# Optimization experiments

Hardware: AMD Instinct MI355X
Metric: run time of the kernel (lower is better)

Reference implementation:

```python
import jax, jax.numpy as jnp
import numpy as np

T, G = 8, 128                      # time frames, spatial grid per axis
RMIN, RMAX = -1.5, 1.5             # same range for x, y, z
STEP = (RMAX - RMIN) / G           # voxel step per axis
# corner order: [C000, C100, C010, C110, C001, C101, C011, C111]
_OFFSETS = jnp.array([[0,0,0],[1,0,0],[0,1,0],[1,1,0],
                      [0,0,1],[1,0,1],[0,1,1],[1,1,1]], dtype=jnp.int32)

def _trilinear_coef(p):
    # p: [N,3] fractional position inside the cell, in [0,1)
    u, v, w = p[:, 0], p[:, 1], p[:, 2]
    return jnp.stack([(1-u)*(1-v)*(1-w), u*(1-v)*(1-w), (1-u)*v*(1-w), u*v*(1-w),
                      (1-u)*(1-v)*w,     u*(1-v)*w,     (1-u)*v*w,     u*v*w], axis=1)

def setup_inputs() -> dict:
    key = jax.random.key(0)
    k1, k2, k3, k4 = jax.random.split(key, 4)
    N = 1048576
    pos = jax.random.uniform(k1, (N, 3), jnp.float32, RMIN, RMAX)
    t = jax.random.randint(k2, (N,), 0, T, dtype=jnp.int32)
    sigma = jax.random.uniform(k3, (N,), jnp.float32)
    target_norm = jax.random.normal(k4, (N, 3), jnp.float32)
    lr = jnp.full((1,), 0.1, jnp.float32)
    voxel_array = jnp.full((T, G, G, G, 3), jnp.sqrt(1.0 / 3.0), jnp.float32)
    return {"t": t, "pos": pos, "lr": lr, "sigma": sigma,
            "target_norm": target_norm, "voxel_array": voxel_array}

def reference(t, pos, lr, sigma, target_norm, voxel_array):
    # shift into [0, range) coords (all axes share the same range/step)
    pos_s = pos - RMIN
    min_idx = jnp.floor(pos_s / STEP).astype(jnp.int32)          # [N,3], == // in source
    idx = jnp.clip(min_idx[:, None, :] + _OFFSETS[None], 0, G - 1)  # [N,8,3]
    frac = jnp.mod(pos_s, STEP) / STEP                           # [N,3]
    coef = _trilinear_coef(frac)                                 # [N,8]
    xi, yi, zi = idx[..., 0], idx[..., 1], idx[..., 2]
    ti = jnp.broadcast_to(t[:, None], xi.shape)                  # [N,8]
    vertex_values = voxel_array[ti, xi, yi, zi]                  # [N,8,3] gather
    value = jnp.sum(coef[:, :, None] * vertex_values, axis=1)    # [N,3]
    # update weights
    sigma_weight = (1.0 - jnp.exp(-sigma))[:, None]              # [N,1]
    update_lambda = jax.nn.sigmoid(lr * sigma_weight * coef)[..., None]  # [N,8,1]
    new_vertex_values = update_lambda * target_norm[:, None, :] + (1.0 - update_lambda) * vertex_values
    diff = new_vertex_values - vertex_values                     # [N,8,3]
    new_voxel = voxel_array.at[ti.reshape(-1), xi.reshape(-1),
                               yi.reshape(-1), zi.reshape(-1)].add(diff.reshape(-1, 3))
    return value, new_voxel
```

## Files before the change

### kernel.cpp

```cpp
#include <hip/hip_runtime.h>
#include <hip/hip_fp16.h>
#include <math.h>


#define GRES 128
#define NBINS (8 * 128 * 128)
#define CAP 16
#define OVF_MAX 16384
#define SCAN_BLOCKS 512
constexpr float RMIN_F = -1.5f;
constexpr float STEP_F = 3.0f / 128.0f;

typedef float f32x4a4 __attribute__((ext_vector_type(4), aligned(4)));
typedef float f32x2a4 __attribute__((ext_vector_type(2), aligned(4)));

__device__ __forceinline__ float fast_sigmoid(float x) {
    if (__builtin_expect(fabsf(x) < 0.5f, 1)) {
        return fmaf(x, fmaf(x * x, -(1.0f / 48.0f), 0.25f), 0.5f);
    }
    return 1.0f / (1.0f + __expf(-x));
}

__device__ __forceinline__ uint4 make_payload(
    int i, float px, float py, float pz, int mz,
    const float* __restrict__ target, float lrsw)
{
    float u = fmodf(px, STEP_F) / STEP_F;
    float v = fmodf(py, STEP_F) / STEP_F;
    float w = fmodf(pz, STEP_F) / STEP_F;
    unsigned qu = (unsigned)(u * 2047.0f + 0.5f);
    unsigned qv = (unsigned)(v * 2047.0f + 0.5f);
    unsigned qw = (unsigned)(w * 1023.0f + 0.5f);
    unsigned hx = (unsigned)__half_as_ushort(__float2half(target[3 * i + 0]));
    unsigned hy = (unsigned)__half_as_ushort(__float2half(target[3 * i + 1]));
    unsigned hz = (unsigned)__half_as_ushort(__float2half(target[3 * i + 2]));
    unsigned hl = (unsigned)__half_as_ushort(__float2half(lrsw));
    uint4 p;
    p.x = (qu << 21) | (qv << 10) | qw;
    p.y = ((unsigned)i << 7) | (unsigned)mz;
    p.z = hx | (hy << 16);
    p.w = hz | (hl << 16);
    return p;
}

__global__ __launch_bounds__(256) void place_kernel(
    const int*   __restrict__ t,     const float* __restrict__ pos,
    const float* __restrict__ lr_p,  const float* __restrict__ sigma,
    const float* __restrict__ target,
    unsigned* __restrict__ hist,     uint4* __restrict__ bins,
    unsigned* __restrict__ ovfcnt,   unsigned* __restrict__ ovf_key,
    uint4*    __restrict__ ovf_pay,  int N)
{
    int i = blockIdx.x * blockDim.x + threadIdx.x;
    if (i >= N) return;
    float px = pos[3 * i + 0] - RMIN_F;
    float py = pos[3 * i + 1] - RMIN_F;
    float pz = pos[3 * i + 2] - RMIN_F;
    int cx = min((int)floorf(px / STEP_F), GRES - 1);
    int cy = min((int)floorf(py / STEP_F), GRES - 1);
    int mz = min((int)floorf(pz / STEP_F), GRES - 1);
    float lrsw = lr_p[0] * (1.0f - __expf(-sigma[i]));
    uint4 p = make_payload(i, px, py, pz, mz, target, lrsw);
    unsigned key  = ((unsigned)t[i] << 14) | ((unsigned)cx << 7) | (unsigned)cy;
    unsigned rank = atomicAdd(&hist[key], 1u);
    if (rank < CAP) {
        bins[(size_t)key * CAP + rank] = p;
    } else {
        unsigned o = atomicAdd(ovfcnt, 1u);
        if (o < OVF_MAX) { ovf_key[o] = key; ovf_pay[o] = p; }
    }
}

__global__ __launch_bounds__(256) void key_hist_kernel(
    const int* __restrict__ t, const float* __restrict__ pos,
    unsigned* __restrict__ keys, unsigned* __restrict__ hist, int N)
{
    int i = blockIdx.x * blockDim.x + threadIdx.x;
    if (i >= N) return;
    float px = pos[3 * i + 0] - RMIN_F;
    float py = pos[3 * i + 1] - RMIN_F;
    int cx = min((int)floorf(px / STEP_F), GRES - 1);
    int cy = min((int)floorf(py / STEP_F), GRES - 1);
    unsigned key  = ((unsigned)t[i] << 14) | ((unsigned)cx << 7) | (unsigned)cy;
    unsigned rank = atomicAdd(&hist[key], 1u);
    keys[i] = (key << 15) | rank;
}

__global__ __launch_bounds__(256) void scanA_kernel(
    const unsigned* __restrict__ hist, unsigned* __restrict__ binstart,
    unsigned* __restrict__ partial)
{
    __shared__ unsigned sh[256];
    const int tid = threadIdx.x;
    const int gid = blockIdx.x * 256 + tid;
    unsigned x = hist[gid];
    sh[tid] = x;
    __syncthreads();
    for (int off = 1; off < 256; off <<= 1) {
        unsigned v = (tid >= off) ? sh[tid - off] : 0u;
        __syncthreads();
        sh[tid] += v;
        __syncthreads();
    }
    binstart[gid] = sh[tid] - x;
    if (tid == 255) partial[blockIdx.x] = sh[255];
}

__global__ __launch_bounds__(256) void scanC_kernel(
    unsigned* __restrict__ binstart, const unsigned* __restrict__ partial, int N)
{
    __shared__ unsigned s_w[4];
    unsigned loc = 0;
    for (int i = threadIdx.x; i < blockIdx.x; i += 256) loc += partial[i];
    #pragma unroll
    for (int off = 32; off > 0; off >>= 1) loc += __shfl_down(loc, off);
    if ((threadIdx.x & 63) == 0) s_w[threadIdx.x >> 6] = loc;
    __syncthreads();
    const unsigned off0 = s_w[0] + s_w[1] + s_w[2] + s_w[3];
    const int gid = blockIdx.x * 256 + threadIdx.x;
    binstart[gid] += off0;
    if (gid == 0) binstart[NBINS] = (unsigned)N;
}

__global__ __launch_bounds__(256) void scatter_kernel(
    const float* __restrict__ pos, const float* __restrict__ lr_p,
    const float* __restrict__ sigma, const float* __restrict__ target,
    const unsigned* __restrict__ keys, const unsigned* __restrict__ binstart,
    uint4* __restrict__ sorted, int N)
{
    int i = blockIdx.x * blockDim.x + threadIdx.x;
    if (i >= N) return;
    unsigned kr   = keys[i];
    unsigned key  = kr >> 15;
    unsigned rank = kr & 0x7fffu;
    unsigned slot = binstart[key] + rank;
    float px = pos[3 * i + 0] - RMIN_F;
    float py = pos[3 * i + 1] - RMIN_F;
    float pz = pos[3 * i + 2] - RMIN_F;
    int   mz = min((int)floorf(pz / STEP_F), GRES - 1);
    float lrsw = lr_p[0] * (1.0f - __expf(-sigma[i]));
    sorted[slot] = make_payload(i, px, py, pz, mz, target, lrsw);
}

__device__ __forceinline__ void process_event(
    const uint4 p, const int cx, const int cy,
    const int x0, const int y0, const int z0, const size_t tbase,
    const float* __restrict__ voxel_in,
    float* __restrict__ out_value, float* __restrict__ s_acc)
{
    const float u = (float)(p.x >> 21)           * (1.0f / 2047.0f);
    const float v = (float)((p.x >> 10) & 2047u) * (1.0f / 2047.0f);
    const float w = (float)(p.x & 1023u)         * (1.0f / 1023.0f);
    const int  mz  = (int)(p.y & 127u);
    const int  idx = (int)(p.y >> 7);
    const float tx = __half2float(__ushort_as_half((unsigned short)(p.z & 0xffffu)));
    const float ty = __half2float(__ushort_as_half((unsigned short)(p.z >> 16)));
    const float tz = __half2float(__ushort_as_half((unsigned short)(p.w & 0xffffu)));
    const float lrsw = __half2float(__ushort_as_half((unsigned short)(p.w >> 16)));

    const int xs1 = min(cx + 1, GRES - 1);
    const int ys1 = min(cy + 1, GRES - 1);
    const int zs1 = min(mz + 1, GRES - 1);
    const int zb  = min(mz, GRES - 2);
    const bool ztop = (mz == GRES - 1);
    const int szl = mz  - z0;
    const int szh = zs1 - z0;

    float lo[4][3], hi[4][3];
    #pragma unroll
    for (int q = 0; q < 4; ++q) {
        const int xi = (q & 1) ? xs1 : cx;
        const int yi = (q & 2) ? ys1 : cy;
        const float* vp = voxel_in + tbase + (((size_t)xi * GRES + yi) * GRES + zb) * 3;
        f32x4a4 f0 = *(const f32x4a4*)vp;
        f32x2a4 f1 = *(const f32x2a4*)(vp + 4);
        hi[q][0] = f0.w; hi[q][1] = f1.x; hi[q][2] = f1.y;
        lo[q][0] = ztop ? f0.w : f0.x;
        lo[q][1] = ztop ? f1.x : f0.y;
        lo[q][2] = ztop ? f1.y : f0.z;
    }

    float c[8];
    c[0] = (1.f - u) * (1.f - v) * (1.f - w);
    c[1] =        u  * (1.f - v) * (1.f - w);
    c[2] = (1.f - u) *        v  * (1.f - w);
    c[3] =        u  *        v  * (1.f - w);
    c[4] = (1.f - u) * (1.f - v) *        w;
    c[5] =        u  * (1.f - v) *        w;
    c[6] = (1.f - u) *        v  *        w;
    c[7] =        u  *        v  *        w;

    const bool owner = (cx >= x0) && (cy >= y0);

    float vx = 0.f, vy = 0.f, vz = 0.f;
    #pragma unroll
    for (int q = 0; q < 4; ++q) {
        if (owner) {
            vx += c[q] * lo[q][0] + c[q + 4] * hi[q][0];
            vy += c[q] * lo[q][1] + c[q + 4] * hi[q][1];
            vz += c[q] * lo[q][2] + c[q + 4] * hi[q][2];
        }
        const int xi = (q & 1) ? xs1 : cx;
        const int yi = (q & 2) ? ys1 : cy;
        const int sxi = xi - x0, syi = yi - y0;
        if (sxi >= 0 && sxi < 4 && syi >= 0 && syi < 4) {
            const int col = (sxi * 4 + syi) * 64;
            if (szl >= 0 && szl < 64) {
                const float laml = fast_sigmoid(lrsw * c[q]);
                const int sal = (col + szl) * 3;
                atomicAdd(&s_acc[sal + 0], laml * (tx - lo[q][0]));
                atomicAdd(&s_acc[sal + 1], laml * (ty - lo[q][1]));
                atomicAdd(&s_acc[sal + 2], laml * (tz - lo[q][2]));
            }
            if (szh >= 0 && szh < 64) {
                const float lamh = fast_sigmoid(lrsw * c[q + 4]);
                const int sah = (col + szh) * 3;
                atomicAdd(&s_acc[sah + 0], lamh * (tx - hi[q][0]));
                atomicAdd(&s_acc[sah + 1], lamh * (ty - hi[q][1]));
                atomicAdd(&s_acc[sah + 2], lamh * (tz - hi[q][2]));
            }
        }
    }
    if (owner) {
        out_value[3 * idx + 0] = vx;
        out_value[3 * idx + 1] = vy;
        out_value[3 * idx + 2] = vz;
    }
}

__global__ __launch_bounds__(256, 8) void brick_kernel(
    const unsigned* __restrict__ counts,
    const uint4*    __restrict__ sorted,
    const float*    __restrict__ voxel_in,
    float*          __restrict__ out_value,
    float*          __restrict__ out_voxel,
    int cap,
    const unsigned* __restrict__ ovf_key,
    const uint4*    __restrict__ ovf_pay,
    const unsigned* __restrict__ ovfcnt)
{
    __shared__ __align__(16) float s_acc[4 * 4 * 64 * 3];
    __shared__ unsigned s_start[25];
    __shared__ unsigned s_pref[26];
    __shared__ unsigned s_novf;

    const int t  = blockIdx.x & 7;
    const int s  = blockIdx.x >> 3;
    const int bx = s >> 6;
    const int by = (s >> 1) & 31;
    const int zh = s & 1;
    const int x0 = bx << 2, y0 = by << 2, z0 = zh << 6;
    const int zlo = z0 ? z0 - 1 : 0;
    const int zhi = z0 + 63;
    const int tid = threadIdx.x;
    const size_t tbase = (size_t)t * (GRES * GRES * GRES * 3);

    float4* s_acc4 = (float4*)s_acc;
    for (int q = tid; q < 768; q += 256) s_acc4[q] = make_float4(0.f, 0.f, 0.f, 0.f);

    if (tid < 64) {
        unsigned st = 0, cnt = 0;
        if (tid < 25) {
            int dxb = tid / 5 - 1, dyb = tid % 5 - 1;
            int cx = x0 + dxb, cy = y0 + dyb;
            if (cx >= 0 && cx < GRES && cy >= 0 && cy < GRES) {
                unsigned key = ((unsigned)t << 14) | ((unsigned)cx << 7) | (unsigned)cy;
                if (cap > 0) {
                    st  = key * (unsigned)cap;
                    cnt = min(counts[key], (unsigned)cap);
                } else {
                    st  = counts[key];
                    cnt = counts[key + 1] - st;
                }
            }
            s_start[tid] = st;
        }
        unsigned x = cnt;
        #pragma unroll
        for (int off = 1; off < 32; off <<= 1) {
            unsigned y = __shfl_up(x, off);
            if (tid >= off) x += y;
        }
        if (tid < 25) s_pref[tid + 1] = x;
        if (tid == 0) s_pref[0] = 0;
    }
    if (tid == 64) s_novf = (cap > 0) ? *ovfcnt : 0u;
    __syncthreads();
    const int P = (int)s_pref[25];

    for (int j = tid; j < P; j += 256) {
        int b = 0;
        #pragma unroll
        for (int sh = 16; sh > 0; sh >>= 1) {
            int nb = b + sh;
            if (nb <= 24 && s_pref[nb] <= (unsigned)j) b = nb;
        }
        const int cx = x0 + b / 5 - 1, cy = y0 + b % 5 - 1;
        const unsigned g = s_start[b] + ((unsigned)j - s_pref[b]);
        const uint4 p = sorted[g];
        const int mz = (int)(p.y & 127u);
        if (mz < zlo || mz > zhi) continue;
        process_event(p, cx, cy, x0, y0, z0, tbase, voxel_in, out_value, s_acc);
    }

    if (cap > 0) {
        const unsigned novf = min(s_novf, (unsigned)OVF_MAX);
        for (unsigned o = tid; o < novf; o += 256) {
            const unsigned key = ovf_key[o];
            if ((int)(key >> 14) != t) continue;
            const int ocx = (int)((key >> 7) & 127u), ocy = (int)(key & 127u);
            const int dxb = ocx - x0, dyb = ocy - y0;
            if (dxb < -1 || dxb > 3 || dyb < -1 || dyb > 3) continue;
            const uint4 p = ovf_pay[o];
            const int mz = (int)(p.y & 127u);
            if (mz < zlo || mz > zhi) continue;
            process_event(p, ocx, ocy, x0, y0, z0, tbase, voxel_in, out_value, s_acc);
        }
    }
    __syncthreads();

    for (int q = tid; q < 768; q += 256) {
        int col = q / 48, r = q - col * 48;
        int ox = col >> 2, oy = col & 3;
        const size_t coff = tbase + (size_t)(x0 + ox) * 49152
                                  + (size_t)(y0 + oy) * 384 + (size_t)z0 * 3;
        float4 a = *((const float4*)(voxel_in + coff) + r);
        float4 d = s_acc4[q];
        *((float4*)(out_voxel + coff) + r) =
            make_float4(a.x + d.x, a.y + d.y, a.z + d.z, a.w + d.w);
    }
}

extern "C" void kernel_launch(void* const* d_in, const int* in_sizes, int n_in,
                              void* d_out, int out_size, void* d_ws, size_t ws_size,
                              hipStream_t stream) {
    const int*   t      = (const int*)  d_in[0];
    const float* pos    = (const float*)d_in[1];
    const float* lr     = (const float*)d_in[2];
    const float* sigma  = (const float*)d_in[3];
    const float* target = (const float*)d_in[4];
    const float* voxel  = (const float*)d_in[5];

    const int N = in_sizes[0];

    float* out_value = (float*)d_out;
    float* out_voxel = out_value + (size_t)3 * N;

    const int block = 256;
    const int grid  = (N + block - 1) / block;

    const size_t need = (size_t)NBINS * CAP * 16 + (size_t)NBINS * 4 + 64
                      + (size_t)OVF_MAX * 4 + (size_t)OVF_MAX * 16;

    if (ws_size >= need) {
        uint4*    bins    = (uint4*)d_ws;
        unsigned* hist    = (unsigned*)(bins + (size_t)NBINS * CAP);
        unsigned* ovfcnt  = hist + NBINS;
        unsigned* ovf_key = ovfcnt + 16;
        uint4*    ovf_pay = (uint4*)(ovf_key + OVF_MAX);

        hipMemsetAsync(hist, 0, NBINS * sizeof(unsigned) + 64, stream);
        place_kernel<<<grid, block, 0, stream>>>(t, pos, lr, sigma, target,
                                                 hist, bins, ovfcnt, ovf_key,
                                                 ovf_pay, N);
        brick_kernel<<<16384, 256, 0, stream>>>(hist, bins, voxel,
                                                out_value, out_voxel,
                                                CAP, ovf_key, ovf_pay, ovfcnt);
    } else {
        uint4*    sorted   = (uint4*)d_ws;
        unsigned* keys     = (unsigned*)(sorted + (size_t)N);
        unsigned* hist     = keys + N;
        unsigned* binstart = hist + NBINS;
        unsigned* partial  = binstart + (NBINS + 1);

        hipMemsetAsync(hist, 0, NBINS * sizeof(unsigned), stream);
        key_hist_kernel<<<grid, block, 0, stream>>>(t, pos, keys, hist, N);
        scanA_kernel<<<SCAN_BLOCKS, 256, 0, stream>>>(hist, binstart, partial);
        scanC_kernel<<<SCAN_BLOCKS, 256, 0, stream>>>(binstart, partial, N);
        scatter_kernel<<<grid, block, 0, stream>>>(pos, lr, sigma, target, keys,
                                                   binstart, sorted, N);
        brick_kernel<<<16384, 256, 0, stream>>>(binstart, sorted, voxel,
                                                out_value, out_voxel,
                                                0, nullptr, nullptr, nullptr);
    }
}
```

Measured before the change: 510.1 us.

## Bin by z-half with 4-byte slot payloads and reload inputs in brick kernel

Bins are split by z-half, so each brick reads only its own events, and events at the z boundary (mz==63) are placed in both halves. Instead of a 16-byte packed payload, each bin entry is now a 4-byte index+mz word. The brick kernel re-reads pos, target and sigma per event, which removes the quantisation and half-precision packing. The multi-kernel sort fallback and the workspace size check are removed, and nontemporal loads and stores are added. This trades smaller bin traffic and exact inputs for random gathers of input arrays in the brick kernel, and it now assumes the workspace is large enough.

After: 546.3 us. +7.1%, slower.

```diff
diff --git a/kernel.cpp b/kernel.cpp
--- a/kernel.cpp
+++ b/kernel.cpp
@@ -4,10 +4,9 @@
 
 
 #define GRES 128
-#define NBINS (8 * 128 * 128)
-#define CAP 16
-#define OVF_MAX 16384
-#define SCAN_BLOCKS 512
+#define NBINS2 (1 << 18)
+#define CAP 12
+#define OVF_MAX 8192
 constexpr float RMIN_F = -1.5f;
 constexpr float STEP_F = 3.0f / 128.0f;
 
@@ -21,35 +20,11 @@
     return 1.0f / (1.0f + __expf(-x));
 }
 
-__device__ __forceinline__ uint4 make_payload(
-    int i, float px, float py, float pz, int mz,
-    const float* __restrict__ target, float lrsw)
-{
-    float u = fmodf(px, STEP_F) / STEP_F;
-    float v = fmodf(py, STEP_F) / STEP_F;
-    float w = fmodf(pz, STEP_F) / STEP_F;
-    unsigned qu = (unsigned)(u * 2047.0f + 0.5f);
-    unsigned qv = (unsigned)(v * 2047.0f + 0.5f);
-    unsigned qw = (unsigned)(w * 1023.0f + 0.5f);
-    unsigned hx = (unsigned)__half_as_ushort(__float2half(target[3 * i + 0]));
-    unsigned hy = (unsigned)__half_as_ushort(__float2half(target[3 * i + 1]));
-    unsigned hz = (unsigned)__half_as_ushort(__float2half(target[3 * i + 2]));
-    unsigned hl = (unsigned)__half_as_ushort(__float2half(lrsw));
-    uint4 p;
-    p.x = (qu << 21) | (qv << 10) | qw;
-    p.y = ((unsigned)i << 7) | (unsigned)mz;
-    p.z = hx | (hy << 16);
-    p.w = hz | (hl << 16);
-    return p;
-}
-
 __global__ __launch_bounds__(256) void place_kernel(
-    const int*   __restrict__ t,     const float* __restrict__ pos,
-    const float* __restrict__ lr_p,  const float* __restrict__ sigma,
-    const float* __restrict__ target,
-    unsigned* __restrict__ hist,     uint4* __restrict__ bins,
-    unsigned* __restrict__ ovfcnt,   unsigned* __restrict__ ovf_key,
-    uint4*    __restrict__ ovf_pay,  int N)
+    const int*  __restrict__ t,    const float* __restrict__ pos,
+    unsigned*   __restrict__ hist, unsigned*    __restrict__ bins,
+    unsigned*   __restrict__ ovfcnt, unsigned*  __restrict__ ovf_key,
+    unsigned*   __restrict__ ovf_slot, int N)
 {
     int i = blockIdx.x * blockDim.x + threadIdx.x;
     if (i >= N) return;
@@ -59,104 +34,38 @@
     int cx = min((int)floorf(px / STEP_F), GRES - 1);
     int cy = min((int)floorf(py / STEP_F), GRES - 1);
     int mz = min((int)floorf(pz / STEP_F), GRES - 1);
-    float lrsw = lr_p[0] * (1.0f - __expf(-sigma[i]));
-    uint4 p = make_payload(i, px, py, pz, mz, target, lrsw);
-    unsigned key  = ((unsigned)t[i] << 14) | ((unsigned)cx << 7) | (unsigned)cy;
-    unsigned rank = atomicAdd(&hist[key], 1u);
+    unsigned slotw = ((unsigned)i << 7) | (unsigned)mz;
+    unsigned key2 = ((((unsigned)t[i] << 14) | ((unsigned)cx << 7)
+                      | (unsigned)cy) << 1) | ((unsigned)mz >> 6);
+    unsigned rank = atomicAdd(&hist[key2], 1u);
     if (rank < CAP) {
-        bins[(size_t)key * CAP + rank] = p;
+        __builtin_nontemporal_store(slotw, &bins[key2 * CAP + rank]);
     } else {
         unsigned o = atomicAdd(ovfcnt, 1u);
-        if (o < OVF_MAX) { ovf_key[o] = key; ovf_pay[o] = p; }
-    }
-}
-
-__global__ __launch_bounds__(256) void key_hist_kernel(
-    const int* __restrict__ t, const float* __restrict__ pos,
-    unsigned* __restrict__ keys, unsigned* __restrict__ hist, int N)
+        if (o < OVF_MAX) { ovf_key[o] = key2; ovf_slot[o] = slotw; }
+    }
+    if (mz == 63) {
+        unsigned k2 = key2 + 1;
+        unsigned r2 = atomicAdd(&hist[k2], 1u);
+        if (r2 < CAP) {
+            __builtin_nontemporal_store(slotw, &bins[k2 * CAP + r2]);
+        } else {
+            unsigned o = atomicAdd(ovfcnt, 1u);
+            if (o < OVF_MAX) { ovf_key[o] = k2; ovf_slot[o] = slotw; }
+        }
+    }
+}
+
+__device__ __forceinline__ void process_event(
+    const unsigned slotw, const int cx, const int cy,
+    const int x0, const int y0, const int z0, const size_t tbase,
+    const float lr0,
+    const float* __restrict__ pos,   const float* __restrict__ target,
+    const float* __restrict__ sigma, const float* __restrict__ voxel_in,
+    float* __restrict__ out_value,   float* __restrict__ s_acc)
 {
-    int i = blockIdx.x * blockDim.x + threadIdx.x;
-    if (i >= N) return;
-    float px = pos[3 * i + 0] - RMIN_F;
-    float py = pos[3 * i + 1] - RMIN_F;
-    int cx = min((int)floorf(px / STEP_F), GRES - 1);
-    int cy = min((int)floorf(py / STEP_F), GRES - 1);
-    unsigned key  = ((unsigned)t[i] << 14) | ((unsigned)cx << 7) | (unsigned)cy;
-    unsigned rank = atomicAdd(&hist[key], 1u);
-    keys[i] = (key << 15) | rank;
-}
-
-__global__ __launch_bounds__(256) void scanA_kernel(
-    const unsigned* __restrict__ hist, unsigned* __restrict__ binstart,
-    unsigned* __restrict__ partial)
-{
-    __shared__ unsigned sh[256];
-    const int tid = threadIdx.x;
-    const int gid = blockIdx.x * 256 + tid;
-    unsigned x = hist[gid];
-    sh[tid] = x;
-    __syncthreads();
-    for (int off = 1; off < 256; off <<= 1) {
-        unsigned v = (tid >= off) ? sh[tid - off] : 0u;
-        __syncthreads();
-        sh[tid] += v;
-        __syncthreads();
-    }
-    binstart[gid] = sh[tid] - x;
-    if (tid == 255) partial[blockIdx.x] = sh[255];
-}
-
-__global__ __launch_bounds__(256) void scanC_kernel(
-    unsigned* __restrict__ binstart, const unsigned* __restrict__ partial, int N)
-{
-    __shared__ unsigned s_w[4];
-    unsigned loc = 0;
-    for (int i = threadIdx.x; i < blockIdx.x; i += 256) loc += partial[i];
-    #pragma unroll
-    for (int off = 32; off > 0; off >>= 1) loc += __shfl_down(loc, off);
-    if ((threadIdx.x & 63) == 0) s_w[threadIdx.x >> 6] = loc;
-    __syncthreads();
-    const unsigned off0 = s_w[0] + s_w[1] + s_w[2] + s_w[3];
-    const int gid = blockIdx.x * 256 + threadIdx.x;
-    binstart[gid] += off0;
-    if (gid == 0) binstart[NBINS] = (unsigned)N;
-}
-
-__global__ __launch_bounds__(256) void scatter_kernel(
-    const float* __restrict__ pos, const float* __restrict__ lr_p,
-    const float* __restrict__ sigma, const float* __restrict__ target,
-    const unsigned* __restrict__ keys, const unsigned* __restrict__ binstart,
-    uint4* __restrict__ sorted, int N)
-{
-    int i = blockIdx.x * blockDim.x + threadIdx.x;
-    if (i >= N) return;
-    unsigned kr   = keys[i];
-    unsigned key  = kr >> 15;
-    unsigned rank = kr & 0x7fffu;
-    unsigned slot = binstart[key] + rank;
-    float px = pos[3 * i + 0] - RMIN_F;
-    float py = pos[3 * i + 1] - RMIN_F;
-    float pz = pos[3 * i + 2] - RMIN_F;
-    int   mz = min((int)floorf(pz / STEP_F), GRES - 1);
-    float lrsw = lr_p[0] * (1.0f - __expf(-sigma[i]));
-    sorted[slot] = make_payload(i, px, py, pz, mz, target, lrsw);
-}
-
-__device__ __forceinline__ void process_event(
-    const uint4 p, const int cx, const int cy,
-    const int x0, const int y0, const int z0, const size_t tbase,
-    const float* __restrict__ voxel_in,
-    float* __restrict__ out_value, float* __restrict__ s_acc)
-{
-    const float u = (float)(p.x >> 21)           * (1.0f / 2047.0f);
-    const float v = (float)((p.x >> 10) & 2047u) * (1.0f / 2047.0f);
-    const float w = (float)(p.x & 1023u)         * (1.0f / 1023.0f);
-    const int  mz  = (int)(p.y & 127u);
-    const int  idx = (int)(p.y >> 7);
-    const float tx = __half2float(__ushort_as_half((unsigned short)(p.z & 0xffffu)));
-    const float ty = __half2float(__ushort_as_half((unsigned short)(p.z >> 16)));
-    const float tz = __half2float(__ushort_as_half((unsigned short)(p.w & 0xffffu)));
-    const float lrsw = __half2float(__ushort_as_half((unsigned short)(p.w >> 16)));
+    const int mz  = (int)(slotw & 127u);
+    const int idx = (int)(slotw >> 7);
 
     const int xs1 = min(cx + 1, GRES - 1);
     const int ys1 = min(cy + 1, GRES - 1);
@@ -179,6 +88,17 @@
         lo[q][1] = ztop ? f1.x : f0.y;
         lo[q][2] = ztop ? f1.y : f0.z;
     }
+    f32x2a4 pxy = *(const f32x2a4*)&pos[3 * idx];
+    float    pzv = pos[3 * idx + 2];
+    f32x2a4 txy = *(const f32x2a4*)&target[3 * idx];
+    float    tzv = target[3 * idx + 2];
+    float    sg  = sigma[idx];
+
+    const float u = fmodf(pxy.x - RMIN_F, STEP_F) / STEP_F;
+    const float v = fmodf(pxy.y - RMIN_F, STEP_F) / STEP_F;
+    const float w = fmodf(pzv   - RMIN_F, STEP_F) / STEP_F;
+    const float tx = txy.x, ty = txy.y, tz = tzv;
+    const float lrsw = lr0 * (1.0f - __expf(-sg));
 
     float c[8];
     c[0] = (1.f - u) * (1.f - v) * (1.f - w);
@@ -222,21 +142,24 @@
         }
     }
     if (owner) {
-        out_value[3 * idx + 0] = vx;
-        out_value[3 * idx + 1] = vy;
-        out_value[3 * idx + 2] = vz;
+        __builtin_nontemporal_store(vx, &out_value[3 * idx + 0]);
+        __builtin_nontemporal_store(vy, &out_value[3 * idx + 1]);
+        __builtin_nontemporal_store(vz, &out_value[3 * idx + 2]);
     }
 }
 
 __global__ __launch_bounds__(256, 8) void brick_kernel(
-    const unsigned* __restrict__ counts,
-    const uint4*    __restrict__ sorted,
+    const unsigned* __restrict__ hist,
+    const unsigned* __restrict__ bins,
+    const float*    __restrict__ pos,
+    const float*    __restrict__ target,
+    const float*    __restrict__ sigma,
+    const float*    __restrict__ lr_p,
     const float*    __restrict__ voxel_in,
     float*          __restrict__ out_value,
     float*          __restrict__ out_voxel,
-    int cap,
     const unsigned* __restrict__ ovf_key,
-    const uint4*    __restrict__ ovf_pay,
+    const unsigned* __restrict__ ovf_slot,
     const unsigned* __restrict__ ovfcnt)
 {
     __shared__ __align__(16) float s_acc[4 * 4 * 64 * 3];
@@ -250,10 +173,9 @@
     const int by = (s >> 1) & 31;
     const int zh = s & 1;
     const int x0 = bx << 2, y0 = by << 2, z0 = zh << 6;
-    const int zlo = z0 ? z0 - 1 : 0;
-    const int zhi = z0 + 63;
     const int tid = threadIdx.x;
     const size_t tbase = (size_t)t * (GRES * GRES * GRES * 3);
+    const float lr0 = lr_p[0];
 
     float4* s_acc4 = (float4*)s_acc;
     for (int q = tid; q < 768; q += 256) s_acc4[q] = make_float4(0.f, 0.f, 0.f, 0.f);
@@ -264,14 +186,10 @@
             int dxb = tid / 5 - 1, dyb = tid % 5 - 1;
             int cx = x0 + dxb, cy = y0 + dyb;
             if (cx >= 0 && cx < GRES && cy >= 0 && cy < GRES) {
-                unsigned key = ((unsigned)t << 14) | ((unsigned)cx << 7) | (unsigned)cy;
-                if (cap > 0) {
-                    st  = key * (unsigned)cap;
-                    cnt = min(counts[key], (unsigned)cap);
-                } else {
-                    st  = counts[key];
-                    cnt = counts[key + 1] - st;
-                }
+                unsigned key2 = ((((unsigned)t << 14) | ((unsigned)cx << 7)
+                                  | (unsigned)cy) << 1) | (unsigned)zh;
+                st  = key2 * CAP;
+                cnt = min(hist[key2], (unsigned)CAP);
             }
             s_start[tid] = st;
         }
@@ -284,7 +202,7 @@
         if (tid < 25) s_pref[tid + 1] = x;
         if (tid == 0) s_pref[0] = 0;
     }
-    if (tid == 64) s_novf = (cap > 0) ? *ovfcnt : 0u;
+    if (tid == 64) s_novf = *ovfcnt;
     __syncthreads();
     const int P = (int)s_pref[25];
 
@@ -297,24 +215,23 @@
         }
         const int cx = x0 + b / 5 - 1, cy = y0 + b % 5 - 1;
         const unsigned g = s_start[b] + ((unsigned)j - s_pref[b]);
-        const uint4 p = sorted[g];
-        const int mz = (int)(p.y & 127u);
-        if (mz < zlo || mz > zhi) continue;
-        process_event(p, cx, cy, x0, y0, z0, tbase, voxel_in, out_value, s_acc);
-    }
-
-    if (cap > 0) {
+        const unsigned slotw = __builtin_nontemporal_load(&bins[g]);
+        process_event(slotw, cx, cy, x0, y0, z0, tbase, lr0,
+                      pos, target, sigma, voxel_in, out_value, s_acc);
+    }
+
+    {
         const unsigned novf = min(s_novf, (unsigned)OVF_MAX);
         for (unsigned o = tid; o < novf; o += 256) {
-            const unsigned key = ovf_key[o];
-            if ((int)(key >> 14) != t) continue;
-            const int ocx = (int)((key >> 7) & 127u), ocy = (int)(key & 127u);
+            const unsigned k2 = ovf_key[o];
+            if ((int)(k2 & 1u) != zh) continue;
+            if ((int)(k2 >> 15) != t) continue;
+            const int ocx = (int)((k2 >> 8) & 127u);
+            const int ocy = (int)((k2 >> 1) & 127u);
             const int dxb = ocx - x0, dyb = ocy - y0;
             if (dxb < -1 || dxb > 3 || dyb < -1 || dyb > 3) continue;
-            const uint4 p = ovf_pay[o];
-            const int mz = (int)(p.y & 127u);
-            if (mz < zlo || mz > zhi) continue;
-            process_event(p, ocx, ocy, x0, y0, z0, tbase, voxel_in, out_value, s_acc);
+            process_event(ovf_slot[o], ocx, ocy, x0, y0, z0, tbase, lr0,
+                          pos, target, sigma, voxel_in, out_value, s_acc);
         }
     }
     __syncthreads();
@@ -346,41 +263,19 @@
     float* out_value = (float*)d_out;
     float* out_voxel = out_value + (size_t)3 * N;
 
+    unsigned* bins     = (unsigned*)d_ws;
+    unsigned* hist     = bins + (size_t)NBINS2 * CAP;
+    unsigned* ovfcnt   = hist + NBINS2;
+    unsigned* ovf_key  = ovfcnt + 16;
+    unsigned* ovf_slot = ovf_key + OVF_MAX;
+
     const int block = 256;
     const int grid  = (N + block - 1) / block;
 
-    const size_t need = (size_t)NBINS * CAP * 16 + (size_t)NBINS * 4 + 64
-                      + (size_t)OVF_MAX * 4 + (size_t)OVF_MAX * 16;
-
-    if (ws_size >= need) {
-        uint4*    bins    = (uint4*)d_ws;
-        unsigned* hist    = (unsigned*)(bins + (size_t)NBINS * CAP);
-        unsigned* ovfcnt  = hist + NBINS;
-        unsigned* ovf_key = ovfcnt + 16;
-        uint4*    ovf_pay = (uint4*)(ovf_key + OVF_MAX);
-
-        hipMemsetAsync(hist, 0, NBINS * sizeof(unsigned) + 64, stream);
-        place_kernel<<<grid, block, 0, stream>>>(t, pos, lr, sigma, target,
-                                                 hist, bins, ovfcnt, ovf_key,
-                                                 ovf_pay, N);
-        brick_kernel<<<16384, 256, 0, stream>>>(hist, bins, voxel,
-                                                out_value, out_voxel,
-                                                CAP, ovf_key, ovf_pay, ovfcnt);
-    } else {
-        uint4*    sorted   = (uint4*)d_ws;
-        unsigned* keys     = (unsigned*)(sorted + (size_t)N);
-        unsigned* hist     = keys + N;
-        unsigned* binstart = hist + NBINS;
-        unsigned* partial  = binstart + (NBINS + 1);
-
-        hipMemsetAsync(hist, 0, NBINS * sizeof(unsigned), stream);
-        key_hist_kernel<<<grid, block, 0, stream>>>(t, pos, keys, hist, N);
-        scanA_kernel<<<SCAN_BLOCKS, 256, 0, stream>>>(hist, binstart, partial);
-        scanC_kernel<<<SCAN_BLOCKS, 256, 0, stream>>>(binstart, partial, N);
-        scatter_kernel<<<grid, block, 0, stream>>>(pos, lr, sigma, target, keys,
-                                                   binstart, sorted, N);
-        brick_kernel<<<16384, 256, 0, stream>>>(binstart, sorted, voxel,
-                                                out_value, out_voxel,
-                                                0, nullptr, nullptr, nullptr);
-    }
-}
+    hipMemsetAsync(hist, 0, NBINS2 * sizeof(unsigned) + 64, stream);
+    place_kernel<<<grid, block, 0, stream>>>(t, pos, hist, bins,
+                                             ovfcnt, ovf_key, ovf_slot, N);
+    brick_kernel<<<16384, 256, 0, stream>>>(hist, bins, pos, target, sigma,
+                                            lr, voxel, out_value, out_voxel,
+                                            ovf_key, ovf_slot, ovfcnt);
+}
```
